# Optimization experiments

Measured on AMD Instinct MI355X. Metric: run time of the kernel, lower is better.

The kernel has to match this reference:

```python
import jax, jax.numpy as jnp
import numpy as np

MAX_LANES = 5
DELTA_V = 1.0
DELTA_D = 6.0


def setup_inputs() -> dict:
    key = jax.random.key(0)
    k1, k2 = jax.random.split(key)
    targets = jax.random.randint(k1, (32, 360, 640), 0, 6, dtype=jnp.int32)
    embedding_vector = jax.random.normal(k2, (32, 4, 360, 640), dtype=jnp.float32)
    return {"targets": targets, "embedding_vector": embedding_vector}


def reference(targets, embedding_vector):
    B, C, H, W = embedding_vector.shape
    L = MAX_LANES
    P = H * W
    t = targets.reshape(B, P)                      # [B,P] labels 0..L
    e = embedding_vector.reshape(B, C, P)          # [B,C,P]

    # per-(batch, lane) segment counts and means
    onehot = (t[:, None, :] == jnp.arange(1, L + 1, dtype=t.dtype)[None, :, None])  # [B,L,P]
    counts = onehot.sum(-1)                        # [B,L] int
    valid = counts > 1                             # lane used only if >1 points
    sums = jnp.einsum('blp,bcp->blc', onehot.astype(e.dtype), e)   # [B,L,C]
    means = sums / jnp.maximum(counts, 1)[..., None].astype(e.dtype)  # [B,L,C]

    # ---- variance (pull) loss: per-point distance to its lane mean ----
    means_ext = jnp.concatenate([jnp.zeros((B, 1, C), e.dtype), means], axis=1)  # [B,L+1,C]
    mean_pix = jnp.take_along_axis(means_ext, t[..., None].astype(jnp.int32), axis=1)  # [B,P,C]
    diff = e.transpose(0, 2, 1) - mean_pix         # [B,P,C]
    sq = jnp.sum(diff * diff, axis=-1)             # [B,P]
    dist = jnp.sqrt(jnp.maximum(sq, 1e-12))
    valid_ext = jnp.concatenate([jnp.zeros((B, 1), bool), valid], axis=1)  # [B,L+1]
    pix_valid = jnp.take_along_axis(valid_ext, t.astype(jnp.int32), axis=1)  # [B,P]
    hinge = jax.nn.relu(dist - DELTA_V)
    dist_sum = jnp.sum(jnp.where(pix_valid, hinge * hinge, 0.0))
    point_count = jnp.sum(jnp.where(valid, counts, 0)).astype(e.dtype)
    dist_loss = jnp.where(point_count > 0, dist_sum / jnp.maximum(point_count, 1.0), 0.0)

    # ---- distance (push) loss: pdist over valid lane means per batch ----
    d = means[:, :, None, :] - means[:, None, :, :]          # [B,L,L,C]
    psq = jnp.sum(d * d, axis=-1)                            # [B,L,L]
    pd = jnp.sqrt(jnp.maximum(psq, 1e-12))
    iu = jnp.arange(L)
    pair_mask = valid[:, :, None] & valid[:, None, :] & (iu[:, None] < iu[None, :])  # [B,L,L]
    ph = jax.nn.relu(DELTA_D - pd)
    per_batch_sum = jnp.sum(jnp.where(pair_mask, ph * ph, 0.0), axis=(1, 2))  # [B]
    npairs = pair_mask.sum((1, 2)).astype(e.dtype)           # [B]
    batch_has = npairs > 0                                   # needs >=2 valid lanes
    var_b = jnp.where(batch_has, per_batch_sum / jnp.maximum(npairs, 1.0), 0.0)
    n_batches = batch_has.sum().astype(e.dtype)
    var_loss = jnp.where(n_batches > 0, var_b.sum() / jnp.maximum(n_batches, 1.0), 0.0)

    return dist_loss + var_loss
```

## Files before the change

### kernel.cpp

```cpp
#include <hip/hip_runtime.h>
#include <math.h>

#define B 32
#define C 4
#define P (360*640)
#define L 5
#define DELTA_V 1.0f
#define DELTA_D 6.0f

#define BLKX 45
#define ITER1 5
#define NBLK3 (B*BLKX)
#define PSTRIDE 48

__device__ __forceinline__ float waveReduce(float v) {
#pragma unroll
    for (int off = 32; off; off >>= 1) v += __shfl_down(v, off, 64);
    return v;
}

__global__ __launch_bounds__(256, 4) void seg_sums_k(const int* __restrict__ tgt,
                                                     const float* __restrict__ emb,
                                                     float* __restrict__ partial) {
    const int xb = blockIdx.x, cp = blockIdx.y, b = blockIdx.z;
    const int tid = threadIdx.x;
    const int c0 = 2 * cp;

    const int4*   t4  = (const int4*)(tgt + (size_t)b * P);
    const float4* ea  = (const float4*)(emb + ((size_t)b * C + c0    ) * P);
    const float4* eb  = (const float4*)(emb + ((size_t)b * C + c0 + 1) * P);

    float s0[L], s1[L], n[L];
#pragma unroll
    for (int l = 0; l < L; ++l) { s0[l] = 0.f; s1[l] = 0.f; n[l] = 0.f; }

    auto acc1 = [&](int tt, float x0, float x1) {
#pragma unroll
        for (int l = 0; l < L; ++l) {
            float m = (tt == l + 1) ? 1.0f : 0.0f;
            n[l]  += m;
            s0[l]  = fmaf(m, x0, s0[l]);
            s1[l]  = fmaf(m, x1, s1[l]);
        }
    };
    auto consume = [&](const int4& tv, const float4& va, const float4& vb) {
        acc1(tv.x, va.x, vb.x);
        acc1(tv.y, va.y, vb.y);
        acc1(tv.z, va.z, vb.z);
        acc1(tv.w, va.w, vb.w);
    };

    int g = xb * 256 + tid;
    int4   ta = t4[g];
    float4 pa = ea[g], pb = eb[g];
#pragma unroll
    for (int it = 0; it < ITER1 - 1; ++it) {
        const int gn = (xb + (it + 1) * BLKX) * 256 + tid;
        int4   tb = t4[gn];
        float4 qa = ea[gn], qb = eb[gn];
        consume(ta, pa, pb);
        ta = tb; pa = qa; pb = qb;
    }
    consume(ta, pa, pb);

    float vals[15];
#pragma unroll
    for (int l = 0; l < L; ++l) { vals[l] = s0[l]; vals[L + l] = s1[l]; vals[10 + l] = n[l]; }

    __shared__ float red[4][15];
    const int lane = tid & 63, wave = tid >> 6;
#pragma unroll
    for (int k = 0; k < 15; ++k) {
        float r = waveReduce(vals[k]);
        if (lane == 0) red[wave][k] = r;
    }
    __syncthreads();
    if (tid < 15) {
        const float r = red[0][tid] + red[1][tid] + red[2][tid] + red[3][tid];
        int v;
        if (cp == 0) v = (tid < 10) ? tid : (tid + 10);
        else         v = (tid < 10) ? (10 + tid) : -1;
        if (v >= 0)
            partial[((size_t)b * 25 + v) * PSTRIDE + xb] = r;
    }
}

__global__ __launch_bounds__(256, 4) void pull_k(const int* __restrict__ tgt,
                                                 const float* __restrict__ emb,
                                                 const float* __restrict__ partial,
                                                 float* __restrict__ meansG,
                                                 float* __restrict__ validG,
                                                 float* __restrict__ cntvG,
                                                 float* __restrict__ pullp) {
    __shared__ float  praw[25];
    __shared__ float4 lmean[L + 1];
    __shared__ float  lvalid[L + 1];
    __shared__ float  lred[4];
    const int xb = blockIdx.x, b = blockIdx.y;
    const int tid = threadIdx.x;
    const int lane = tid & 63, wave = tid >> 6;

    for (int v = wave; v < 25; v += 4) {
        float pv = (lane < BLKX) ? partial[((size_t)b * 25 + v) * PSTRIDE + lane] : 0.f;
        pv = waveReduce(pv);
        if (lane == 0) praw[v] = pv;
    }
    __syncthreads();
    if (tid < L) {
        const float cnt = praw[20 + tid];
        const bool  vld = cnt > 1.5f;
        const float inv = 1.0f / fmaxf(cnt, 1.0f);
        float4 m = make_float4(praw[tid] * inv, praw[5 + tid] * inv,
                               praw[10 + tid] * inv, praw[15 + tid] * inv);
        lmean[tid + 1]  = m;
        lvalid[tid + 1] = vld ? 1.f : 0.f;
        if (xb == 0) {
            *(float4*)(meansG + ((size_t)b * L + tid) * 4) = m;
            validG[b * L + tid] = vld ? 1.f : 0.f;
            cntvG[b * L + tid]  = vld ? cnt : 0.f;
        }
    }
    if (tid == 8) { lmean[0] = make_float4(0.f, 0.f, 0.f, 0.f); lvalid[0] = 0.f; }
    __syncthreads();

    const int4*   t4 = (const int4*)(tgt + (size_t)b * P);
    const float4* e0 = (const float4*)(emb + ((size_t)b * C + 0) * P);
    const float4* e1 = (const float4*)(emb + ((size_t)b * C + 1) * P);
    const float4* e2 = (const float4*)(emb + ((size_t)b * C + 2) * P);
    const float4* e3 = (const float4*)(emb + ((size_t)b * C + 3) * P);

    float acc = 0.f;
    auto proc1 = [&](int tt, float v0, float v1, float v2, float v3) {
        float4 m = lmean[tt];
        float d0 = v0 - m.x, d1 = v1 - m.y, d2 = v2 - m.z, d3 = v3 - m.w;
        float sq   = d0*d0 + d1*d1 + d2*d2 + d3*d3;
        float dist = sqrtf(fmaxf(sq, 1e-12f));
        float h    = fmaxf(dist - DELTA_V, 0.f);
        acc = fmaf(lvalid[tt] * h, h, acc);
    };

    int g = xb * 256 + tid;
    int4   ta = t4[g];
    float4 p0 = e0[g], p1 = e1[g], p2 = e2[g], p3 = e3[g];
#pragma unroll
    for (int it = 0; it < ITER1 - 1; ++it) {
        const int gn = (xb + (it + 1) * BLKX) * 256 + tid;
        int4   tb = t4[gn];
        float4 q0 = e0[gn], q1 = e1[gn], q2 = e2[gn], q3 = e3[gn];
        proc1(ta.x, p0.x, p1.x, p2.x, p3.x);
        proc1(ta.y, p0.y, p1.y, p2.y, p3.y);
        proc1(ta.z, p0.z, p1.z, p2.z, p3.z);
        proc1(ta.w, p0.w, p1.w, p2.w, p3.w);
        ta = tb; p0 = q0; p1 = q1; p2 = q2; p3 = q3;
    }
    proc1(ta.x, p0.x, p1.x, p2.x, p3.x);
    proc1(ta.y, p0.y, p1.y, p2.y, p3.y);
    proc1(ta.z, p0.z, p1.z, p2.z, p3.z);
    proc1(ta.w, p0.w, p1.w, p2.w, p3.w);

    float r = waveReduce(acc);
    if (lane == 0) lred[wave] = r;
    __syncthreads();
    if (tid == 0)
        pullp[b * BLKX + xb] = lred[0] + lred[1] + lred[2] + lred[3];
}

__global__ __launch_bounds__(256) void finish_k(const float* __restrict__ pullp,
                                                const float* __restrict__ meansG,
                                                const float* __restrict__ validG,
                                                const float* __restrict__ cntvG,
                                                float* __restrict__ out) {
    __shared__ float red[4][4];
    const int tid = threadIdx.x;
    const int lane = tid & 63, wave = tid >> 6;

    float vb = 0.f, has = 0.f;
    if (tid < B) {
        const float* mb = meansG + tid * L * 4;
        const float* vv = validG + tid * L;
        float ssum = 0.f, np = 0.f;
#pragma unroll
        for (int i = 0; i < L; ++i)
#pragma unroll
            for (int j = i + 1; j < L; ++j) {
                float ok = vv[i] * vv[j];
                float d0 = mb[i*4+0] - mb[j*4+0];
                float d1 = mb[i*4+1] - mb[j*4+1];
                float d2 = mb[i*4+2] - mb[j*4+2];
                float d3 = mb[i*4+3] - mb[j*4+3];
                float psq = d0*d0 + d1*d1 + d2*d2 + d3*d3;
                float pd  = sqrtf(fmaxf(psq, 1e-12f));
                float ph  = fmaxf(DELTA_D - pd, 0.f);
                ssum += ok * ph * ph;
                np   += ok;
            }
        if (np > 0.f) { vb = ssum / np; has = 1.f; }
    }
    float pc = (tid < B*L) ? cntvG[tid] : 0.f;
    float ps = 0.f;
    for (int i = tid; i < NBLK3; i += 256) ps += pullp[i];

    float rvb = waveReduce(vb);
    float rhs = waveReduce(has);
    float rpc = waveReduce(pc);
    float rps = waveReduce(ps);
    if (lane == 0) { red[wave][0]=rvb; red[wave][1]=rhs; red[wave][2]=rpc; red[wave][3]=rps; }
    __syncthreads();
    if (tid == 0) {
        float svb = red[0][0]+red[1][0]+red[2][0]+red[3][0];
        float shs = red[0][1]+red[1][1]+red[2][1]+red[3][1];
        float spc = red[0][2]+red[1][2]+red[2][2]+red[3][2];
        float sps = red[0][3]+red[1][3]+red[2][3]+red[3][3];
        float var = (shs > 0.f) ? svb / shs : 0.f;
        float dl  = (spc > 0.f) ? sps / fmaxf(spc, 1.f) : 0.f;
        out[0] = dl + var;
    }
}

extern "C" void kernel_launch(void* const* d_in, const int* in_sizes, int n_in,
                              void* d_out, int out_size, void* d_ws, size_t ws_size,
                              hipStream_t stream) {
    const int*   tgt = (const int*)d_in[0];
    const float* emb = (const float*)d_in[1];

    float* ws      = (float*)d_ws;
    float* partial = ws;
    float* meansG  = partial + (size_t)B*25*PSTRIDE;
    float* validG  = meansG + (size_t)B*L*4;
    float* cntvG   = validG + B*L;
    float* pullp   = cntvG + B*L;

    seg_sums_k<<<dim3(BLKX, 2, B), 256, 0, stream>>>(tgt, emb, partial);
    pull_k<<<dim3(BLKX, B), 256, 0, stream>>>(tgt, emb, partial,
                                              meansG, validG, cntvG, pullp);
    finish_k<<<1, 256, 0, stream>>>(pullp, meansG, validG, cntvG, (float*)d_out);
}
```

Before: 257.2 us.

## Split segment sums per channel and pack labels to bytes for pull pass

```diff
diff --git a/kernel.cpp b/kernel.cpp
--- a/kernel.cpp
+++ b/kernel.cpp
@@ -21,71 +21,75 @@
 
 __global__ __launch_bounds__(256, 4) void seg_sums_k(const int* __restrict__ tgt,
                                                      const float* __restrict__ emb,
-                                                     float* __restrict__ partial) {
-    const int xb = blockIdx.x, cp = blockIdx.y, b = blockIdx.z;
+                                                     float* __restrict__ partial,
+                                                     unsigned char* __restrict__ tpk) {
+    const int x = blockIdx.x, c = blockIdx.y, b = blockIdx.z;
     const int tid = threadIdx.x;
-    const int c0 = 2 * cp;
-
-    const int4*   t4  = (const int4*)(tgt + (size_t)b * P);
-    const float4* ea  = (const float4*)(emb + ((size_t)b * C + c0    ) * P);
-    const float4* eb  = (const float4*)(emb + ((size_t)b * C + c0 + 1) * P);
-
-    float s0[L], s1[L], n[L];
-#pragma unroll
-    for (int l = 0; l < L; ++l) { s0[l] = 0.f; s1[l] = 0.f; n[l] = 0.f; }
-
-    auto acc1 = [&](int tt, float x0, float x1) {
+
+    const int4*   t4 = (const int4*)(tgt + (size_t)b * P);
+    const float4* ec = (const float4*)(emb + ((size_t)b * C + c) * P);
+
+    int4   tv[ITER1];
+    float4 ev[ITER1];
+#pragma unroll
+    for (int it = 0; it < ITER1; ++it) {
+        const int g = (x + it * BLKX) * 256 + tid;
+        tv[it] = t4[g];
+        ev[it] = ec[g];
+    }
+
+    if (c == 0) {
+        uchar4* tp4 = (uchar4*)(tpk + (size_t)b * P);
+#pragma unroll
+        for (int it = 0; it < ITER1; ++it) {
+            const int g = (x + it * BLKX) * 256 + tid;
+            tp4[g] = make_uchar4((unsigned char)tv[it].x, (unsigned char)tv[it].y,
+                                 (unsigned char)tv[it].z, (unsigned char)tv[it].w);
+        }
+    }
+
+    float s[L], n[L];
+#pragma unroll
+    for (int l = 0; l < L; ++l) { s[l] = 0.f; n[l] = 0.f; }
+
+    auto acc1 = [&](int tt, float e) {
 #pragma unroll
         for (int l = 0; l < L; ++l) {
             float m = (tt == l + 1) ? 1.0f : 0.0f;
-            n[l]  += m;
-            s0[l]  = fmaf(m, x0, s0[l]);
-            s1[l]  = fmaf(m, x1, s1[l]);
+            n[l] += m;
+            s[l] = fmaf(m, e, s[l]);
         }
     };
-    auto consume = [&](const int4& tv, const float4& va, const float4& vb) {
-        acc1(tv.x, va.x, vb.x);
-        acc1(tv.y, va.y, vb.y);
-        acc1(tv.z, va.z, vb.z);
-        acc1(tv.w, va.w, vb.w);
-    };
-
-    int g = xb * 256 + tid;
-    int4   ta = t4[g];
-    float4 pa = ea[g], pb = eb[g];
-#pragma unroll
-    for (int it = 0; it < ITER1 - 1; ++it) {
-        const int gn = (xb + (it + 1) * BLKX) * 256 + tid;
-        int4   tb = t4[gn];
-        float4 qa = ea[gn], qb = eb[gn];
-        consume(ta, pa, pb);
-        ta = tb; pa = qa; pb = qb;
-    }
-    consume(ta, pa, pb);
-
-    float vals[15];
-#pragma unroll
-    for (int l = 0; l < L; ++l) { vals[l] = s0[l]; vals[L + l] = s1[l]; vals[10 + l] = n[l]; }
-
-    __shared__ float red[4][15];
+#pragma unroll
+    for (int it = 0; it < ITER1; ++it) {
+        acc1(tv[it].x, ev[it].x);
+        acc1(tv[it].y, ev[it].y);
+        acc1(tv[it].z, ev[it].z);
+        acc1(tv[it].w, ev[it].w);
+    }
+
+    float vals[2*L];
+#pragma unroll
+    for (int l = 0; l < L; ++l) { vals[l] = s[l]; vals[L + l] = n[l]; }
+
+    __shared__ float red[4][2*L];
     const int lane = tid & 63, wave = tid >> 6;
 #pragma unroll
-    for (int k = 0; k < 15; ++k) {
+    for (int k = 0; k < 2*L; ++k) {
         float r = waveReduce(vals[k]);
         if (lane == 0) red[wave][k] = r;
     }
     __syncthreads();
-    if (tid < 15) {
+    if (tid < L) {
         const float r = red[0][tid] + red[1][tid] + red[2][tid] + red[3][tid];
-        int v;
-        if (cp == 0) v = (tid < 10) ? tid : (tid + 10);
-        else         v = (tid < 10) ? (10 + tid) : -1;
-        if (v >= 0)
-            partial[((size_t)b * 25 + v) * PSTRIDE + xb] = r;
-    }
-}
-
-__global__ __launch_bounds__(256, 4) void pull_k(const int* __restrict__ tgt,
+        partial[((size_t)b * 25 + c * L + tid) * PSTRIDE + x] = r;
+    } else if (c == 0 && tid < 2*L) {
+        const float r = red[0][tid] + red[1][tid] + red[2][tid] + red[3][tid];
+        partial[((size_t)b * 25 + 20 + (tid - L)) * PSTRIDE + x] = r;
+    }
+}
+
+__global__ __launch_bounds__(256, 4) void pull_k(const unsigned char* __restrict__ tpk,
                                                  const float* __restrict__ emb,
                                                  const float* __restrict__ partial,
                                                  float* __restrict__ meansG,
@@ -123,11 +127,11 @@
     if (tid == 8) { lmean[0] = make_float4(0.f, 0.f, 0.f, 0.f); lvalid[0] = 0.f; }
     __syncthreads();
 
-    const int4*   t4 = (const int4*)(tgt + (size_t)b * P);
-    const float4* e0 = (const float4*)(emb + ((size_t)b * C + 0) * P);
-    const float4* e1 = (const float4*)(emb + ((size_t)b * C + 1) * P);
-    const float4* e2 = (const float4*)(emb + ((size_t)b * C + 2) * P);
-    const float4* e3 = (const float4*)(emb + ((size_t)b * C + 3) * P);
+    const uchar4* tp4 = (const uchar4*)(tpk + (size_t)b * P);
+    const float4* e0  = (const float4*)(emb + ((size_t)b * C + 0) * P);
+    const float4* e1  = (const float4*)(emb + ((size_t)b * C + 1) * P);
+    const float4* e2  = (const float4*)(emb + ((size_t)b * C + 2) * P);
+    const float4* e3  = (const float4*)(emb + ((size_t)b * C + 3) * P);
 
     float acc = 0.f;
     auto proc1 = [&](int tt, float v0, float v1, float v2, float v3) {
@@ -138,25 +142,36 @@
         float h    = fmaxf(dist - DELTA_V, 0.f);
         acc = fmaf(lvalid[tt] * h, h, acc);
     };
-
-    int g = xb * 256 + tid;
-    int4   ta = t4[g];
-    float4 p0 = e0[g], p1 = e1[g], p2 = e2[g], p3 = e3[g];
-#pragma unroll
-    for (int it = 0; it < ITER1 - 1; ++it) {
-        const int gn = (xb + (it + 1) * BLKX) * 256 + tid;
-        int4   tb = t4[gn];
-        float4 q0 = e0[gn], q1 = e1[gn], q2 = e2[gn], q3 = e3[gn];
-        proc1(ta.x, p0.x, p1.x, p2.x, p3.x);
-        proc1(ta.y, p0.y, p1.y, p2.y, p3.y);
-        proc1(ta.z, p0.z, p1.z, p2.z, p3.z);
-        proc1(ta.w, p0.w, p1.w, p2.w, p3.w);
-        ta = tb; p0 = q0; p1 = q1; p2 = q2; p3 = q3;
-    }
-    proc1(ta.x, p0.x, p1.x, p2.x, p3.x);
-    proc1(ta.y, p0.y, p1.y, p2.y, p3.y);
-    proc1(ta.z, p0.z, p1.z, p2.z, p3.z);
-    proc1(ta.w, p0.w, p1.w, p2.w, p3.w);
+    auto consume = [&](uchar4 t, const float4& a0, const float4& a1,
+                       const float4& a2, const float4& a3) {
+        proc1(t.x, a0.x, a1.x, a2.x, a3.x);
+        proc1(t.y, a0.y, a1.y, a2.y, a3.y);
+        proc1(t.z, a0.z, a1.z, a2.z, a3.z);
+        proc1(t.w, a0.w, a1.w, a2.w, a3.w);
+    };
+
+    {
+        const int g0 = xb * 256 + tid, g1 = (xb + BLKX) * 256 + tid;
+        uchar4 t0 = tp4[g0], t1 = tp4[g1];
+        float4 a0 = e0[g0], a1 = e1[g0], a2 = e2[g0], a3 = e3[g0];
+        float4 b0 = e0[g1], b1 = e1[g1], b2 = e2[g1], b3 = e3[g1];
+        consume(t0, a0, a1, a2, a3);
+        consume(t1, b0, b1, b2, b3);
+    }
+    {
+        const int g0 = (xb + 2*BLKX) * 256 + tid, g1 = (xb + 3*BLKX) * 256 + tid;
+        uchar4 t0 = tp4[g0], t1 = tp4[g1];
+        float4 a0 = e0[g0], a1 = e1[g0], a2 = e2[g0], a3 = e3[g0];
+        float4 b0 = e0[g1], b1 = e1[g1], b2 = e2[g1], b3 = e3[g1];
+        consume(t0, a0, a1, a2, a3);
+        consume(t1, b0, b1, b2, b3);
+    }
+    {
+        const int g0 = (xb + 4*BLKX) * 256 + tid;
+        uchar4 t0 = tp4[g0];
+        float4 a0 = e0[g0], a1 = e1[g0], a2 = e2[g0], a3 = e3[g0];
+        consume(t0, a0, a1, a2, a3);
+    }
 
     float r = waveReduce(acc);
     if (lane == 0) lred[wave] = r;
@@ -223,15 +238,16 @@
     const int*   tgt = (const int*)d_in[0];
     const float* emb = (const float*)d_in[1];
 
-    float* ws      = (float*)d_ws;
-    float* partial = ws;
-    float* meansG  = partial + (size_t)B*25*PSTRIDE;
-    float* validG  = meansG + (size_t)B*L*4;
-    float* cntvG   = validG + B*L;
-    float* pullp   = cntvG + B*L;
-
-    seg_sums_k<<<dim3(BLKX, 2, B), 256, 0, stream>>>(tgt, emb, partial);
-    pull_k<<<dim3(BLKX, B), 256, 0, stream>>>(tgt, emb, partial,
+    unsigned char* tpk = (unsigned char*)d_ws;
+    float* fbase   = (float*)((char*)d_ws + (size_t)B * P);
+    float* partial = fbase;
+    float* meansG  = partial + (size_t)B * 25 * PSTRIDE;
+    float* validG  = meansG + (size_t)B * L * 4;
+    float* cntvG   = validG + B * L;
+    float* pullp   = cntvG + B * L;
+
+    seg_sums_k<<<dim3(BLKX, C, B), 256, 0, stream>>>(tgt, emb, partial, tpk);
+    pull_k<<<dim3(BLKX, B), 256, 0, stream>>>(tpk, emb, partial,
                                               meansG, validG, cntvG, pullp);
     finish_k<<<1, 256, 0, stream>>>(pullp, meansG, validG, cntvG, (float*)d_out);
 }
```

New measurement: 216.9 us. 15.7% less time.
